# Performance work log

Measured on AMD Instinct MI355X. Metric: run time of the kernel, lower is better.

The kernel has to match this reference:

```python
import jax, jax.numpy as jnp
import numpy as np

D_MODEL = 1024
NHEAD = 16
D_HEAD = D_MODEL // NHEAD
DIM_FF = 4096
EPS = 1e-5

def layer_norm(x, scale, bias):
    mu = jnp.mean(x, axis=-1, keepdims=True)
    var = jnp.mean(jnp.square(x - mu), axis=-1, keepdims=True)
    return (x - mu) * jax.lax.rsqrt(var + EPS) * scale + bias

def setup_inputs() -> dict:
    key = jax.random.key(0)
    ks = jax.random.split(key, 8)
    B, T, D = 4, 2048, D_MODEL
    s = 1.0 / np.sqrt(D)
    sf = 1.0 / np.sqrt(DIM_FF)
    return {
        "x": jax.random.normal(ks[0], (B, T, D), dtype=jnp.float32),
        "ln1_scale": jnp.ones((D,), jnp.float32),
        "ln1_bias": jnp.zeros((D,), jnp.float32),
        "qkv_w": jax.random.normal(ks[1], (3 * D, D), jnp.float32) * s,  # torch Linear weight [out,in]
        "out_w": jax.random.normal(ks[2], (D, D), jnp.float32) * s,
        "ln2_scale": jnp.ones((D,), jnp.float32),
        "ln2_bias": jnp.zeros((D,), jnp.float32),
        "fc1_w": jax.random.normal(ks[3], (DIM_FF, D), jnp.float32) * s,
        "fc1_b": jnp.zeros((DIM_FF,), jnp.float32),
        "fc2_w": jax.random.normal(ks[4], (D, DIM_FF), jnp.float32) * sf,
        "fc2_b": jnp.zeros((D,), jnp.float32),
    }

def reference(x, ln1_scale, ln1_bias, qkv_w, out_w, ln2_scale, ln2_bias, fc1_w, fc1_b, fc2_w, fc2_b):
    B, T, D = x.shape
    # --- attention sublayer (pre-LN) ---
    h = layer_norm(x, ln1_scale, ln1_bias)
    qkv = jnp.einsum('btd,ed->bte', h, qkv_w)  # [B,T,3D]
    q, k, v = jnp.split(qkv, 3, axis=-1)
    def heads(t):
        return t.reshape(B, T, NHEAD, D_HEAD).transpose(0, 2, 1, 3)  # [B,H,T,dh]
    q, k, v = heads(q), heads(k), heads(v)
    scores = jnp.einsum('bhqd,bhkd->bhqk', q, k) / np.sqrt(D_HEAD)
    attn = jax.nn.softmax(scores, axis=-1)
    o = jnp.einsum('bhqk,bhkd->bhqd', attn, v)
    o = o.transpose(0, 2, 1, 3).reshape(B, T, D)
    h = jnp.einsum('btd,ed->bte', o, out_w)
    x = x + h
    # --- FFN sublayer (pre-LN) ---
    h = layer_norm(x, ln2_scale, ln2_bias)
    h = jnp.einsum('btd,fd->btf', h, fc1_w) + fc1_b
    h = jax.nn.gelu(h, approximate=False)
    h = jnp.einsum('btf,df->btd', h, fc2_w) + fc2_b
    return x + h
```

## Files before the change

### kernel.cpp

```cpp
#include <hip/hip_runtime.h>
#include <hip/hip_bf16.h>
#include <math.h>

typedef unsigned short u16;
typedef unsigned int u32;
typedef short s8v __attribute__((ext_vector_type(8)));
typedef float f4v __attribute__((ext_vector_type(4)));
typedef float f16v __attribute__((ext_vector_type(16)));
typedef u32 u4v __attribute__((ext_vector_type(4)));
typedef u32 u2v __attribute__((ext_vector_type(2)));

#define D_MODEL 1024
#define DIMFF   4096
#define SEQ     2048
#define TOKENS  8192

#define QSCALE 0.18033688011112042f

static __device__ __forceinline__ u16 f2bf(float f) {
    unsigned int u = __builtin_bit_cast(unsigned int, f);
    unsigned int lsb = (u >> 16) & 1u;
    u += 0x7fffu + lsb;
    return (u16)(u >> 16);
}

static __device__ __forceinline__ float gelu_fast(float z) {
    float z2 = z * z;
    float p  = fmaf(z2, -0.1029472255f, -2.3021867892f);
    float e  = __builtin_amdgcn_exp2f(z * p);
    return z * __builtin_amdgcn_rcpf(1.0f + e);
}

static __device__ __forceinline__ void gl2lds16(const u16* g, u16* l) {
    __builtin_amdgcn_global_load_lds(
        (__attribute__((address_space(1))) void*)(void*)g,
        (__attribute__((address_space(3))) void*)l, 16, 0, 0);
}

static __device__ __forceinline__ void bar() {
    __builtin_amdgcn_sched_barrier(0);
    asm volatile("" ::: "memory");
    __builtin_amdgcn_s_barrier();
    asm volatile("" ::: "memory");
    __builtin_amdgcn_sched_barrier(0);
}

template<int N> static __device__ __forceinline__ void vwait() {
    if constexpr (N == 4)       asm volatile("s_waitcnt vmcnt(4)" ::: "memory");
    else if constexpr (N == 9)  asm volatile("s_waitcnt vmcnt(9)" ::: "memory");
    else if constexpr (N == 12) asm volatile("s_waitcnt vmcnt(12)" ::: "memory");
    else                        asm volatile("s_waitcnt vmcnt(0)" ::: "memory");
}

#define N4_QKV  786432
#define N4_WO   262144
#define N4_FC   1048576
__global__ __launch_bounds__(256) void cvt_all_kernel(const float* __restrict__ s0,
                                                      const float* __restrict__ s1,
                                                      const float* __restrict__ s2,
                                                      const float* __restrict__ s3,
                                                      u16* __restrict__ dst) {
    int i = blockIdx.x * 256 + threadIdx.x;
    const float* src; int j;
    if (i < N4_QKV)                    { src = s0; j = i; }
    else if (i < N4_QKV + N4_WO)       { src = s1; j = i - N4_QKV; }
    else if (i < N4_QKV + N4_WO + N4_FC) { src = s2; j = i - N4_QKV - N4_WO; }
    else                               { src = s3; j = i - N4_QKV - N4_WO - N4_FC; }
    float4 v = ((const float4*)src)[j];
    ushort4 o;
    o.x = f2bf(v.x); o.y = f2bf(v.y); o.z = f2bf(v.z); o.w = f2bf(v.w);
    ((ushort4*)dst)[i] = o;
}

__global__ __launch_bounds__(256) void ln_kernel(const float* __restrict__ x,
                                                 const float* __restrict__ scale,
                                                 const float* __restrict__ bias,
                                                 u16* __restrict__ out) {
    int row = blockIdx.x;
    int t = threadIdx.x;
    const float* xr = x + (size_t)row * D_MODEL;
    float4 v = ((const float4*)xr)[t];
    float s  = v.x + v.y + v.z + v.w;
    float ss = v.x*v.x + v.y*v.y + v.z*v.z + v.w*v.w;
    #pragma unroll
    for (int off = 1; off < 64; off <<= 1) {
        s  += __shfl_xor(s, off);
        ss += __shfl_xor(ss, off);
    }
    __shared__ float red[8];
    int wave = t >> 6, lane = t & 63;
    if (lane == 0) { red[wave] = s; red[4 + wave] = ss; }
    __syncthreads();
    float S  = red[0] + red[1] + red[2] + red[3];
    float SS = red[4] + red[5] + red[6] + red[7];
    float mu  = S * (1.0f / D_MODEL);
    float var = SS * (1.0f / D_MODEL) - mu * mu;
    float r = rsqrtf(var + 1e-5f);
    float4 sc = ((const float4*)scale)[t];
    float4 bi = ((const float4*)bias)[t];
    ushort4 o;
    o.x = f2bf((v.x - mu) * r * sc.x + bi.x);
    o.y = f2bf((v.y - mu) * r * sc.y + bi.y);
    o.z = f2bf((v.z - mu) * r * sc.z + bi.z);
    o.w = f2bf((v.w - mu) * r * sc.w + bi.w);
    ((ushort4*)(out + (size_t)row * D_MODEL))[t] = o;
}

template<int MODE, int DEPTH>
__global__ __launch_bounds__(512, 2) void gemm_kernel(
        const u16* __restrict__ A, const u16* __restrict__ W,
        const float* __restrict__ bias, const float* __restrict__ res,
        void* __restrict__ outp, void* __restrict__ out2, int M, int N, int K) {
    constexpr int BM = 256, BN_ = 128, BK = 32;
    constexpr int RA = 2;
    constexpr int RB = 1;
    constexpr int S = DEPTH - 1;
    constexpr int VST = (S - 2) * (RA + RB);
    constexpr int ASZ = BM * BK, BSZ = BN_ * BK;
    __shared__ __attribute__((aligned(16))) u16 As[DEPTH * ASZ];
    __shared__ __attribute__((aligned(16))) u16 Bs[DEPTH * BSZ];

    int t = threadIdx.x;
    int lane = t & 63, w = t >> 6;
    int lc = lane & 15, lr = lane >> 4;
    int nb = N / BN_;
    int xcd = blockIdx.x & 7, li = blockIdx.x >> 3;
    int bm = xcd * 4 + (li & 3), bn = li >> 2;
    (void)nb;
    int m0 = bm * BM, n0 = bn * BN_;
    int wm = (w & 3) * 64;
    int wn = (w >> 2) * 64;
    int cxor = (lr ^ ((lc >> 1) & 3)) * 8;

    const u16* Abase = A + (size_t)m0 * K;
    const u16* Bbase = W + (size_t)n0 * K;

    size_t aoff[RA]; int aldo[RA];
    #pragma unroll
    for (int n = 0; n < RA; ++n) {
        int q = (n * 8 + w) * 64 + lane;
        int row = q >> 2;
        aoff[n] = (size_t)row * K + (((q & 3) ^ ((row >> 1) & 3)) * 8);
        aldo[n] = (n * 8 + w) * 512;
    }
    size_t boff; int bldo;
    {
        int q = w * 64 + lane;
        int row = q >> 2;
        boff = (size_t)row * K + (((q & 3) ^ ((row >> 1) & 3)) * 8);
        bldo = w * 512;
    }

    const int NT = K / BK;
    for (int u = 0; u < S; ++u) {
        size_t kk = (size_t)u * BK;
        #pragma unroll
        for (int n = 0; n < RA; ++n) gl2lds16(Abase + aoff[n] + kk, &As[u * ASZ + aldo[n]]);
        gl2lds16(Bbase + boff + kk, &Bs[u * BSZ + bldo]);
    }
    vwait<VST>();
    bar();

    f4v acc[4][4] = {};
    s8v afA[4], bA_[4], afB[4], bB_[4];
    #pragma unroll
    for (int i = 0; i < 4; ++i)
        afA[i] = *(const s8v*)&As[(wm + i * 16 + lc) * BK + cxor];
    #pragma unroll
    for (int j = 0; j < 4; ++j)
        bA_[j] = *(const s8v*)&Bs[(wn + j * 16 + lc) * BK + cxor];
    int rs = 1, ss = S;

#define GSTEP(T, AFL, BL, AFC, BC)                                            \
    {                                                                         \
        const u16* Ab = &As[rs * ASZ];                                        \
        const u16* Bb = &Bs[rs * BSZ];                                        \
        _Pragma("unroll")                                                     \
        for (int i = 0; i < 4; ++i)                                           \
            AFL[i] = *(const s8v*)&Ab[(wm + i * 16 + lc) * BK + cxor];        \
        _Pragma("unroll")                                                     \
        for (int j = 0; j < 4; ++j)                                           \
            BL[j] = *(const s8v*)&Bb[(wn + j * 16 + lc) * BK + cxor];         \
        int kts = (T) + S; if (kts > NT - 1) kts = NT - 1;                    \
        size_t kk = (size_t)kts * BK;                                         \
        _Pragma("unroll")                                                     \
        for (int n = 0; n < RA; ++n)                                          \
            gl2lds16(Abase + aoff[n] + kk, &As[ss * ASZ + aldo[n]]);          \
        gl2lds16(Bbase + boff + kk, &Bs[ss * BSZ + bldo]);                    \
        __builtin_amdgcn_s_setprio(1);                                        \
        _Pragma("unroll")                                                     \
        for (int i = 0; i < 4; ++i) {                                         \
            _Pragma("unroll")                                                 \
            for (int j = 0; j < 4; ++j) {                                     \
                if constexpr (MODE == 4)                                      \
                    acc[i][j] = __builtin_amdgcn_mfma_f32_16x16x32_bf16(AFC[i], BC[j], acc[i][j], 0, 0, 0); \
                else                                                          \
                    acc[i][j] = __builtin_amdgcn_mfma_f32_16x16x32_bf16(BC[j], AFC[i], acc[i][j], 0, 0, 0); \
            }                                                                 \
        }                                                                     \
        __builtin_amdgcn_s_setprio(0);                                        \
        vwait<VST>();                                                         \
        bar();                                                                \
        rs = (rs + 1 == DEPTH) ? 0 : rs + 1;                                  \
        ss = (ss + 1 == DEPTH) ? 0 : ss + 1;                                  \
    }

    for (int kt = 0; kt < NT; kt += 2) {
        GSTEP(kt,     afB, bB_, afA, bA_)
        GSTEP(kt + 1, afA, bA_, afB, bB_)
    }
#undef GSTEP

    if constexpr (MODE == 4) {
        #pragma unroll
        for (int i = 0; i < 4; ++i) {
            #pragma unroll
            for (int j = 0; j < 4; ++j) {
                int col = n0 + wn + j * 16 + lc;
                int colbase = n0 + wn + j * 16;
                if (colbase < 2048) {
                    float sc = (colbase < 1024) ? QSCALE : 1.0f;
                    #pragma unroll
                    for (int r = 0; r < 4; ++r) {
                        int row = m0 + wm + i * 16 + lr * 4 + r;
                        ((u16*)outp)[(size_t)row * 2048 + col] = f2bf(acc[i][j][r] * sc);
                    }
                } else {
                    int dlin = col - 2048;
                    int h = dlin >> 6, dd = dlin & 63;
                    int trow = m0 + wm + i * 16 + lr * 4;
                    int bb = trow >> 11, tt = trow & 2047;
                    int bh = bb * 16 + h;
                    ushort4 vv;
                    vv.x = f2bf(acc[i][j][0]); vv.y = f2bf(acc[i][j][1]);
                    vv.z = f2bf(acc[i][j][2]); vv.w = f2bf(acc[i][j][3]);
                    *(ushort4*)&((u16*)out2)[((size_t)bh * 64 + dd) * SEQ + tt] = vv;
                }
            }
        }
    } else {
        #pragma unroll
        for (int j = 0; j < 4; ++j) {
            int colb = n0 + wn + j * 16 + lr * 4;
            float4 b4;
            if constexpr (MODE != 1) b4 = *(const float4*)&bias[colb];
            #pragma unroll
            for (int i = 0; i < 4; ++i) {
                int row = m0 + wm + i * 16 + lc;
                size_t idx = (size_t)row * N + colb;
                f4v a = acc[i][j];
                if constexpr (MODE == 2) {
                    ushort4 o;
                    o.x = f2bf(gelu_fast(a[0] + b4.x));
                    o.y = f2bf(gelu_fast(a[1] + b4.y));
                    o.z = f2bf(gelu_fast(a[2] + b4.z));
                    o.w = f2bf(gelu_fast(a[3] + b4.w));
                    *(ushort4*)&((u16*)outp)[idx] = o;
                } else {
                    float4 rr = *(const float4*)&res[idx];
                    float4 o;
                    if constexpr (MODE == 3) {
                        o.x = rr.x + a[0] + b4.x; o.y = rr.y + a[1] + b4.y;
                        o.z = rr.z + a[2] + b4.z; o.w = rr.w + a[3] + b4.w;
                    } else {
                        o.x = rr.x + a[0]; o.y = rr.y + a[1];
                        o.z = rr.z + a[2]; o.w = rr.w + a[3];
                    }
                    *(float4*)&((float*)outp)[idx] = o;
                }
            }
        }
    }
}

__global__ __launch_bounds__(256) void attn_kernel(const u16* __restrict__ qk,
                                                   const u16* __restrict__ vt,
                                                   u16* __restrict__ out) {
    __shared__ __attribute__((aligned(16))) u16 Ks[64 * 64];
    __shared__ __attribute__((aligned(16))) u16 Vts[64 * 64];
    __shared__ float l_s[128];
    int t = threadIdx.x, lane = t & 63, w = t >> 6;
    int l31 = lane & 31, hi = lane >> 5;
    int blk = blockIdx.x;
    int bh = blk & 63, qt = blk >> 6;
    int b = bh >> 4, h = bh & 15;
    size_t tok0 = (size_t)b * SEQ;
    int q0 = qt * 128;

    s8v bq[4];
    {
        const u16* qp = qk + (tok0 + q0 + w * 32 + l31) * 2048 + h * 64 + hi * 8;
        #pragma unroll
        for (int dch = 0; dch < 4; ++dch) bq[dch] = *(const s8v*)(qp + dch * 16);
    }
    f16v o[2] = {};
    float lp = 0.f;

    int srow[2], scg[2];
    #pragma unroll
    for (int n = 0; n < 2; ++n) {
        int chunk = (w * 2 + n) * 64 + lane;
        srow[n] = chunk >> 3;
        scg[n]  = ((chunk & 7) ^ (srow[n] & 7)) * 8;
    }
    const u16* vbase = vt + (size_t)bh * 64 * SEQ;

    for (int kt = 0; kt < SEQ / 64; ++kt) {
        #pragma unroll
        for (int n = 0; n < 2; ++n) {
            gl2lds16(&qk[(tok0 + kt * 64 + srow[n]) * 2048 + 1024 + h * 64 + scg[n]],
                     &Ks[(w * 2 + n) * 512]);
            gl2lds16(&vbase[(size_t)srow[n] * SEQ + kt * 64 + scg[n]],
                     &Vts[(w * 2 + n) * 512]);
        }
        __syncthreads();

        f16v s_[2] = {};
        #pragma unroll
        for (int kb = 0; kb < 2; ++kb)
            #pragma unroll
            for (int dch = 0; dch < 4; ++dch) {
                s8v ak = *(const s8v*)&Ks[(kb * 32 + l31) * 64 + ((dch * 2 + hi) ^ (l31 & 7)) * 8];
                s_[kb] = __builtin_amdgcn_mfma_f32_32x32x16_bf16(ak, bq[dch], s_[kb], 0, 0, 0);
            }

        u2v pk[2][4];
        #pragma unroll
        for (int kb = 0; kb < 2; ++kb)
            #pragma unroll
            for (int g = 0; g < 4; ++g) {
                u32 ib[4];
                #pragma unroll
                for (int rr = 0; rr < 4; ++rr) {
                    ib[rr] = (u32)fmaf(s_[kb][g * 4 + rr], 8388608.0f, 1064992506.0f);
                    lp += __builtin_bit_cast(float, ib[rr]);
                }
                pk[kb][g][0] = __builtin_amdgcn_perm(ib[1], ib[0], 0x07060302);
                pk[kb][g][1] = __builtin_amdgcn_perm(ib[3], ib[2], 0x07060302);
            }

        #pragma unroll
        for (int ch = 0; ch < 4; ++ch) {
            int kb = ch >> 1, a2 = (ch & 1) * 2;
            u2v sx = __builtin_amdgcn_permlane32_swap(pk[kb][a2][0], pk[kb][a2 + 1][0], false, false);
            u2v sy = __builtin_amdgcn_permlane32_swap(pk[kb][a2][1], pk[kb][a2 + 1][1], false, false);
            u4v tmp; tmp.x = sx[0]; tmp.y = sy[0]; tmp.z = sx[1]; tmp.w = sy[1];
            s8v ap = __builtin_bit_cast(s8v, tmp);
            #pragma unroll
            for (int dblk = 0; dblk < 2; ++dblk) {
                s8v bv = *(const s8v*)&Vts[(dblk * 32 + l31) * 64 + ((ch * 2 + hi) ^ (l31 & 7)) * 8];
                o[dblk] = __builtin_amdgcn_mfma_f32_32x32x16_bf16(ap, bv, o[dblk], 0, 0, 0);
            }
        }
        __syncthreads();
    }

    lp += __shfl_xor(lp, 32);
    l_s[w * 32 + l31] = 1.0f / lp;
    #pragma unroll
    for (int r = 0; r < 16; ++r) {
        int qrl = (r & 3) + 8 * (r >> 2) + 4 * hi;
        float linv = l_s[w * 32 + qrl];
        size_t row = tok0 + q0 + w * 32 + qrl;
        #pragma unroll
        for (int dblk = 0; dblk < 2; ++dblk)
            out[row * 1024 + h * 64 + dblk * 32 + l31] = f2bf(o[dblk][r] * linv);
    }
}

extern "C" void kernel_launch(void* const* d_in, const int* in_sizes, int n_in,
                              void* d_out, int out_size, void* d_ws, size_t ws_size,
                              hipStream_t stream) {
    const float* x      = (const float*)d_in[0];
    const float* ln1_s  = (const float*)d_in[1];
    const float* ln1_b  = (const float*)d_in[2];
    const float* qkv_w  = (const float*)d_in[3];
    const float* out_w  = (const float*)d_in[4];
    const float* ln2_s  = (const float*)d_in[5];
    const float* ln2_b  = (const float*)d_in[6];
    const float* fc1_w  = (const float*)d_in[7];
    const float* fc1_b  = (const float*)d_in[8];
    const float* fc2_w  = (const float*)d_in[9];
    const float* fc2_b  = (const float*)d_in[10];
    float* out = (float*)d_out;

    char* ws = (char*)d_ws;
    size_t off = 0;
    auto alloc = [&](size_t bytes) -> void* {
        void* p = ws + off;
        off += (bytes + 255) & ~(size_t)255;
        return p;
    };
    u16* wq  = (u16*)alloc((size_t)3072 * 1024 * 2);
    u16* wo  = (u16*)alloc((size_t)1024 * 1024 * 2);
    u16* w1  = (u16*)alloc((size_t)4096 * 1024 * 2);
    u16* w2  = (u16*)alloc((size_t)1024 * 4096 * 2);
    u16* h1  = (u16*)alloc((size_t)TOKENS * 1024 * 2);
    u16* qk  = (u16*)alloc((size_t)TOKENS * 2048 * 2);
    float* x2 = (float*)alloc((size_t)TOKENS * 1024 * 4);
    u16* g   = (u16*)alloc((size_t)TOKENS * 4096 * 2);
    u16* attn_out = h1;
    u16* h2       = qk;
    u16* vt       = (u16*)x2;
    (void)wo; (void)w1; (void)w2;

    cvt_all_kernel<<<(N4_QKV + N4_WO + 2 * N4_FC) / 256, 256, 0, stream>>>(
        qkv_w, out_w, fc1_w, fc2_w, wq);

    ln_kernel<<<TOKENS, 256, 0, stream>>>(x, ln1_s, ln1_b, h1);
    gemm_kernel<4, 6><<<(TOKENS / 256) * (3072 / 128), 512, 0, stream>>>(
        h1, wq, nullptr, nullptr, qk, vt, TOKENS, 3072, 1024);
    attn_kernel<<<64 * 16, 256, 0, stream>>>(qk, vt, attn_out);
    gemm_kernel<1, 6><<<(TOKENS / 256) * (1024 / 128), 512, 0, stream>>>(
        attn_out, wo, nullptr, x, x2, nullptr, TOKENS, 1024, 1024);
    ln_kernel<<<TOKENS, 256, 0, stream>>>(x2, ln2_s, ln2_b, h2);
    gemm_kernel<2, 6><<<(TOKENS / 256) * (DIMFF / 128), 512, 0, stream>>>(
        h2, w1, fc1_b, nullptr, g, nullptr, TOKENS, DIMFF, 1024);
    gemm_kernel<3, 6><<<(TOKENS / 256) * (1024 / 128), 512, 0, stream>>>(
        g, w2, fc2_b, x2, out, nullptr, TOKENS, 1024, DIMFF);
}
```

Before: 482.2 us.

## Restructure GEMM main loop into BK=64 triple-buffered four-phase pipeline

```diff
diff --git a/kernel.cpp b/kernel.cpp
--- a/kernel.cpp
+++ b/kernel.cpp
@@ -46,9 +46,8 @@
 }
 
 template<int N> static __device__ __forceinline__ void vwait() {
-    if constexpr (N == 4)       asm volatile("s_waitcnt vmcnt(4)" ::: "memory");
-    else if constexpr (N == 9)  asm volatile("s_waitcnt vmcnt(9)" ::: "memory");
-    else if constexpr (N == 12) asm volatile("s_waitcnt vmcnt(12)" ::: "memory");
+    if constexpr (N == 6)       asm volatile("s_waitcnt vmcnt(6)" ::: "memory");
+    else if constexpr (N == 8)  asm volatile("s_waitcnt vmcnt(8)" ::: "memory");
     else                        asm volatile("s_waitcnt vmcnt(0)" ::: "memory");
 }
 
@@ -106,110 +105,131 @@
     ((ushort4*)(out + (size_t)row * D_MODEL))[t] = o;
 }
 
-template<int MODE, int DEPTH>
+template<int MODE>
 __global__ __launch_bounds__(512, 2) void gemm_kernel(
         const u16* __restrict__ A, const u16* __restrict__ W,
         const float* __restrict__ bias, const float* __restrict__ res,
         void* __restrict__ outp, void* __restrict__ out2, int M, int N, int K) {
-    constexpr int BM = 256, BN_ = 128, BK = 32;
-    constexpr int RA = 2;
-    constexpr int RB = 1;
-    constexpr int S = DEPTH - 1;
-    constexpr int VST = (S - 2) * (RA + RB);
+    constexpr int BM = 256, BN_ = 128, BK = 64;
     constexpr int ASZ = BM * BK, BSZ = BN_ * BK;
-    __shared__ __attribute__((aligned(16))) u16 As[DEPTH * ASZ];
-    __shared__ __attribute__((aligned(16))) u16 Bs[DEPTH * BSZ];
+    __shared__ __attribute__((aligned(16))) u16 As[3][ASZ];
+    __shared__ __attribute__((aligned(16))) u16 Bs[3][BSZ];
 
     int t = threadIdx.x;
     int lane = t & 63, w = t >> 6;
     int lc = lane & 15, lr = lane >> 4;
-    int nb = N / BN_;
     int xcd = blockIdx.x & 7, li = blockIdx.x >> 3;
     int bm = xcd * 4 + (li & 3), bn = li >> 2;
-    (void)nb;
     int m0 = bm * BM, n0 = bn * BN_;
-    int wm = (w & 3) * 64;
-    int wn = (w >> 2) * 64;
-    int cxor = (lr ^ ((lc >> 1) & 3)) * 8;
+    int wm = (w >> 1) * 64, wn = (w & 1) * 64;
 
     const u16* Abase = A + (size_t)m0 * K;
     const u16* Bbase = W + (size_t)n0 * K;
 
-    size_t aoff[RA]; int aldo[RA];
-    #pragma unroll
-    for (int n = 0; n < RA; ++n) {
-        int q = (n * 8 + w) * 64 + lane;
-        int row = q >> 2;
-        aoff[n] = (size_t)row * K + (((q & 3) ^ ((row >> 1) & 3)) * 8);
-        aldo[n] = (n * 8 + w) * 512;
-    }
-    size_t boff; int bldo;
-    {
-        int q = w * 64 + lane;
-        int row = q >> 2;
-        boff = (size_t)row * K + (((q & 3) ^ ((row >> 1) & 3)) * 8);
-        bldo = w * 512;
-    }
-
-    const int NT = K / BK;
-    for (int u = 0; u < S; ++u) {
-        size_t kk = (size_t)u * BK;
-        #pragma unroll
-        for (int n = 0; n < RA; ++n) gl2lds16(Abase + aoff[n] + kk, &As[u * ASZ + aldo[n]]);
-        gl2lds16(Bbase + boff + kk, &Bs[u * BSZ + bldo]);
-    }
-    vwait<VST>();
+    int aoff[4], aldo[4];
+    #pragma unroll
+    for (int a = 0; a < 4; ++a) {
+        int opid = a * 8 + w;
+        int row = opid * 8 + (lane >> 3);
+        aoff[a] = row * K + ((lane & 7) ^ (row & 7)) * 8;
+        aldo[a] = opid * 512;
+    }
+    int boff[2], bldo[2];
+    #pragma unroll
+    for (int b = 0; b < 2; ++b) {
+        int opid = b * 8 + w;
+        int row = opid * 8 + (lane >> 3);
+        boff[b] = row * K + ((lane & 7) ^ (row & 7)) * 8;
+        bldo[b] = opid * 512;
+    }
+
+    const int NK = K / BK;
+    #pragma unroll
+    for (int kk = 0; kk < 2; ++kk) {
+        #pragma unroll
+        for (int a = 0; a < 4; ++a) gl2lds16(Abase + aoff[a] + kk * 64, &As[kk][aldo[a]]);
+        #pragma unroll
+        for (int b = 0; b < 2; ++b) gl2lds16(Bbase + boff[b] + kk * 64, &Bs[kk][bldo[b]]);
+    }
+    vwait<0>();
     bar();
 
     f4v acc[4][4] = {};
-    s8v afA[4], bA_[4], afB[4], bB_[4];
-    #pragma unroll
-    for (int i = 0; i < 4; ++i)
-        afA[i] = *(const s8v*)&As[(wm + i * 16 + lc) * BK + cxor];
-    #pragma unroll
-    for (int j = 0; j < 4; ++j)
-        bA_[j] = *(const s8v*)&Bs[(wn + j * 16 + lc) * BK + cxor];
-    int rs = 1, ss = S;
-
-#define GSTEP(T, AFL, BL, AFC, BC)                                            \
+    s8v af[2][2], bf[2][2];
+    const u16* Ar = As[0];  const u16* Br = Bs[0];
+    u16* An = (u16*)As[1];  u16* Bn = (u16*)Bs[1];
+    u16* Ass = (u16*)As[2]; u16* Bss = (u16*)Bs[2];
+
+#define PH_HEAD(Q)                                                            \
     {                                                                         \
-        const u16* Ab = &As[rs * ASZ];                                        \
-        const u16* Bb = &Bs[rs * BSZ];                                        \
-        _Pragma("unroll")                                                     \
-        for (int i = 0; i < 4; ++i)                                           \
-            AFL[i] = *(const s8v*)&Ab[(wm + i * 16 + lc) * BK + cxor];        \
-        _Pragma("unroll")                                                     \
-        for (int j = 0; j < 4; ++j)                                           \
-            BL[j] = *(const s8v*)&Bb[(wn + j * 16 + lc) * BK + cxor];         \
-        int kts = (T) + S; if (kts > NT - 1) kts = NT - 1;                    \
-        size_t kk = (size_t)kts * BK;                                         \
-        _Pragma("unroll")                                                     \
-        for (int n = 0; n < RA; ++n)                                          \
-            gl2lds16(Abase + aoff[n] + kk, &As[ss * ASZ + aldo[n]]);          \
-        gl2lds16(Bbase + boff + kk, &Bs[ss * BSZ + bldo]);                    \
+        constexpr int ihh = (Q) >> 1;                                         \
+        constexpr int jhh = ((Q) == 1 || (Q) == 2) ? 1 : 0;                   \
+        if constexpr ((Q) == 0 || (Q) == 2) {                                 \
+            _Pragma("unroll")                                                 \
+            for (int i = 0; i < 2; ++i) {                                     \
+                int row = wm + ihh * 32 + i * 16 + lc;                        \
+                _Pragma("unroll")                                             \
+                for (int ks = 0; ks < 2; ++ks)                                \
+                    af[i][ks] = *(const s8v*)&Ar[row * 64 + ((ks * 4 + lr) ^ (row & 7)) * 8]; \
+            }                                                                 \
+        }                                                                     \
+        if constexpr ((Q) != 2) {                                             \
+            _Pragma("unroll")                                                 \
+            for (int j = 0; j < 2; ++j) {                                     \
+                int row = wn + jhh * 32 + j * 16 + lc;                        \
+                _Pragma("unroll")                                             \
+                for (int ks = 0; ks < 2; ++ks)                                \
+                    bf[j][ks] = *(const s8v*)&Br[row * 64 + ((ks * 4 + lr) ^ (row & 7)) * 8]; \
+            }                                                                 \
+        }                                                                     \
+        if (st) {                                                             \
+            if constexpr ((Q) == 0) { gl2lds16(Ag + aoff[0], Ass + aldo[0]);  \
+                                      gl2lds16(Ag + aoff[1], Ass + aldo[1]); }\
+            if constexpr ((Q) == 1) { gl2lds16(Bg + boff[0], Bss + bldo[0]); }\
+            if constexpr ((Q) == 2) { gl2lds16(Ag + aoff[2], Ass + aldo[2]);  \
+                                      gl2lds16(Ag + aoff[3], Ass + aldo[3]); }\
+            if constexpr ((Q) == 3) { gl2lds16(Bg + boff[1], Bss + bldo[1]); }\
+        }                                                                     \
+    }
+
+#define PH_MFMA(Q)                                                            \
+    {                                                                         \
+        constexpr int ihh = (Q) >> 1;                                         \
+        constexpr int jhh = ((Q) == 1 || (Q) == 2) ? 1 : 0;                   \
+        asm volatile("s_waitcnt lgkmcnt(0)" ::: "memory");                    \
+        __builtin_amdgcn_sched_barrier(0);                                    \
         __builtin_amdgcn_s_setprio(1);                                        \
         _Pragma("unroll")                                                     \
-        for (int i = 0; i < 4; ++i) {                                         \
+        for (int i = 0; i < 2; ++i)                                           \
             _Pragma("unroll")                                                 \
-            for (int j = 0; j < 4; ++j) {                                     \
-                if constexpr (MODE == 4)                                      \
-                    acc[i][j] = __builtin_amdgcn_mfma_f32_16x16x32_bf16(AFC[i], BC[j], acc[i][j], 0, 0, 0); \
-                else                                                          \
-                    acc[i][j] = __builtin_amdgcn_mfma_f32_16x16x32_bf16(BC[j], AFC[i], acc[i][j], 0, 0, 0); \
-            }                                                                 \
-        }                                                                     \
+            for (int j = 0; j < 2; ++j)                                       \
+                _Pragma("unroll")                                             \
+                for (int ks = 0; ks < 2; ++ks) {                              \
+                    if constexpr (MODE == 4)                                  \
+                        acc[ihh*2+i][jhh*2+j] = __builtin_amdgcn_mfma_f32_16x16x32_bf16(af[i][ks], bf[j][ks], acc[ihh*2+i][jhh*2+j], 0, 0, 0); \
+                    else                                                      \
+                        acc[ihh*2+i][jhh*2+j] = __builtin_amdgcn_mfma_f32_16x16x32_bf16(bf[j][ks], af[i][ks], acc[ihh*2+i][jhh*2+j], 0, 0, 0); \
+                }                                                             \
         __builtin_amdgcn_s_setprio(0);                                        \
-        vwait<VST>();                                                         \
-        bar();                                                                \
-        rs = (rs + 1 == DEPTH) ? 0 : rs + 1;                                  \
-        ss = (ss + 1 == DEPTH) ? 0 : ss + 1;                                  \
-    }
-
-    for (int kt = 0; kt < NT; kt += 2) {
-        GSTEP(kt,     afB, bB_, afA, bA_)
-        GSTEP(kt + 1, afA, bA_, afB, bB_)
-    }
-#undef GSTEP
+    }
+
+    for (int k = 0; k < NK; ++k) {
+        bool st = (k < NK - 2);
+        const u16* Ag = Abase + (k + 2) * 64;
+        const u16* Bg = Bbase + (k + 2) * 64;
+
+        PH_HEAD(0) bar(); PH_MFMA(0) bar();
+        PH_HEAD(1) bar(); PH_MFMA(1) bar();
+        PH_HEAD(2) bar(); PH_MFMA(2) bar();
+        PH_HEAD(3) bar(); PH_MFMA(3)
+        if (k < NK - 2)      vwait<6>();
+        else if (k == NK - 2) vwait<0>();
+        bar();
+        const u16* tA = Ar; Ar = An; An = Ass; Ass = (u16*)tA;
+        const u16* tB = Br; Br = Bn; Bn = Bss; Bss = (u16*)tB;
+    }
+#undef PH_HEAD
+#undef PH_MFMA
 
     if constexpr (MODE == 4) {
         #pragma unroll
@@ -408,14 +428,14 @@
         qkv_w, out_w, fc1_w, fc2_w, wq);
 
     ln_kernel<<<TOKENS, 256, 0, stream>>>(x, ln1_s, ln1_b, h1);
-    gemm_kernel<4, 6><<<(TOKENS / 256) * (3072 / 128), 512, 0, stream>>>(
+    gemm_kernel<4><<<(TOKENS / 256) * (3072 / 128), 512, 0, stream>>>(
         h1, wq, nullptr, nullptr, qk, vt, TOKENS, 3072, 1024);
     attn_kernel<<<64 * 16, 256, 0, stream>>>(qk, vt, attn_out);
-    gemm_kernel<1, 6><<<(TOKENS / 256) * (1024 / 128), 512, 0, stream>>>(
+    gemm_kernel<1><<<(TOKENS / 256) * (1024 / 128), 512, 0, stream>>>(
         attn_out, wo, nullptr, x, x2, nullptr, TOKENS, 1024, 1024);
     ln_kernel<<<TOKENS, 256, 0, stream>>>(x2, ln2_s, ln2_b, h2);
-    gemm_kernel<2, 6><<<(TOKENS / 256) * (DIMFF / 128), 512, 0, stream>>>(
+    gemm_kernel<2><<<(TOKENS / 256) * (DIMFF / 128), 512, 0, stream>>>(
         h2, w1, fc1_b, nullptr, g, nullptr, TOKENS, DIMFF, 1024);
-    gemm_kernel<3, 6><<<(TOKENS / 256) * (1024 / 128), 512, 0, stream>>>(
+    gemm_kernel<3><<<(TOKENS / 256) * (1024 / 128), 512, 0, stream>>>(
         g, w2, fc2_b, x2, out, nullptr, TOKENS, 1024, DIMFF);
 }
```

New measurement: 512.9 us. 1.06x slower.
